# Optimization experiments

Measured on AMD Instinct MI355X. Metric: run time of the kernel, lower is better.

## Reference

```python
import jax, jax.numpy as jnp
import numpy as np

N_NODES = 100000
N_EDGES = 1000000
NEG_SLOPE = 0.2


def gat_conv(x, src, dst, W, al, ar, b, res, activation):
    """DGL-style GATConv. res is None (no residual), 'id' (identity residual), or a [in,H*D] matrix."""
    H, D = al.shape
    n = x.shape[0]
    feat = (x @ W).reshape(n, H, D)                      # [N,H,D]
    el = jnp.einsum('nhd,hd->nh', feat, al)              # [N,H]
    er = jnp.einsum('nhd,hd->nh', feat, ar)              # [N,H]
    e = jax.nn.leaky_relu(el[src] + er[dst], NEG_SLOPE)  # [E,H]
    # edge softmax over incoming edges of each dst node
    m = jax.lax.stop_gradient(jax.ops.segment_max(e, dst, num_segments=n))
    ex = jnp.exp(e - m[dst])
    s = jax.ops.segment_sum(ex, dst, num_segments=n)
    alpha = ex / s[dst]                                  # [E,H]
    out = jax.ops.segment_sum(feat[src] * alpha[:, :, None], dst, num_segments=n)  # [N,H,D]
    if res == 'id':
        out = out + x.reshape(n, H, D)
    elif res is not None:
        out = out + (x @ res).reshape(n, H, D)
    out = out + b.reshape(1, H, D)
    if activation is not None:
        out = activation(out)
    return out


def setup_inputs() -> dict:
    key = jax.random.key(0)
    ks = jax.random.split(key, 20)
    F_IN, HID = 128, 32
    H1, H2, H3 = 4, 4, 1
    C = 40
    sc = 0.1
    inp = {
        'x':   jax.random.normal(ks[0], (N_NODES, F_IN), dtype=jnp.float32),
        'src': jax.random.randint(ks[1], (N_EDGES,), 0, N_NODES, dtype=jnp.int32),
        'dst': jax.random.randint(ks[2], (N_EDGES,), 0, N_NODES, dtype=jnp.int32),
        # layer 1: in=128 -> H1*HID=128, no residual, elu
        'W1':  sc * jax.random.normal(ks[3], (F_IN, H1 * HID), dtype=jnp.float32),
        'al1': sc * jax.random.normal(ks[4], (H1, HID), dtype=jnp.float32),
        'ar1': sc * jax.random.normal(ks[5], (H1, HID), dtype=jnp.float32),
        'b1':  jnp.zeros((H1 * HID,), dtype=jnp.float32),
        # layer 2: in=128 -> H2*HID=128, identity residual, elu
        'W2':  sc * jax.random.normal(ks[6], (H1 * HID, H2 * HID), dtype=jnp.float32),
        'al2': sc * jax.random.normal(ks[7], (H2, HID), dtype=jnp.float32),
        'ar2': sc * jax.random.normal(ks[8], (H2, HID), dtype=jnp.float32),
        'b2':  jnp.zeros((H2 * HID,), dtype=jnp.float32),
        # layer 3 (output): in=128 -> H3*HID=32, projected residual, no activation
        'W3':  sc * jax.random.normal(ks[9], (H2 * HID, H3 * HID), dtype=jnp.float32),
        'al3': sc * jax.random.normal(ks[10], (H3, HID), dtype=jnp.float32),
        'ar3': sc * jax.random.normal(ks[11], (H3, HID), dtype=jnp.float32),
        'b3':  jnp.zeros((H3 * HID,), dtype=jnp.float32),
        'res3': sc * jax.random.normal(ks[12], (H2 * HID, H3 * HID), dtype=jnp.float32),
        # final classifier
        'Wfc': sc * jax.random.normal(ks[13], (HID, C), dtype=jnp.float32),
        'bfc': jnp.zeros((C,), dtype=jnp.float32),
    }
    return inp


def reference(x, src, dst, W1, al1, ar1, b1, W2, al2, ar2, b2, W3, al3, ar3, b3, res3, Wfc, bfc):
    n = x.shape[0]
    h = gat_conv(x, src, dst, W1, al1, ar1, b1, None, jax.nn.elu).reshape(n, -1)   # [N, 128]
    h = gat_conv(h, src, dst, W2, al2, ar2, b2, 'id', jax.nn.elu).reshape(n, -1)   # [N, 128]
    h = gat_conv(h, src, dst, W3, al3, ar3, b3, res3, None).mean(axis=1)           # [N, 32]
    return h @ Wfc + bfc                                                           # [N, 40]
```

## Files before the change

kernel.cpp:

```cpp
#include <hip/hip_runtime.h>
#include <cstdint>
#include <cstddef>

#define NN 100000
#define NE 1000000

typedef unsigned int uint;
typedef unsigned short ushort;
typedef __attribute__((ext_vector_type(8))) short bfrag;
typedef __attribute__((ext_vector_type(4))) float f32x4;

__device__ __forceinline__ ushort f2bf(float f){
  uint u = __float_as_uint(f);
  u += 0x7fffu + ((u >> 16) & 1u);
  return (ushort)(u >> 16);
}
__device__ __forceinline__ float bflo(uint p){ return __uint_as_float(p << 16); }
__device__ __forceinline__ float bfhi(uint p){ return __uint_as_float(p & 0xffff0000u); }


__global__ __launch_bounds__(256) void k_ticket(const int* __restrict__ dst, int* __restrict__ cnt,
                                                int* __restrict__ tick){
  int e = blockIdx.x*256 + threadIdx.x;
  if (e < NE) tick[e] = atomicAdd(&cnt[dst[e]], 1);
}

__global__ __launch_bounds__(256) void k_scan_local(const int* __restrict__ cnt, int* __restrict__ rowptr,
                                                    int* __restrict__ bsum){
  __shared__ int sm[256];
  int t = threadIdx.x;
  int i = blockIdx.x*256 + t;
  int v = (i < NN) ? cnt[i] : 0;
  sm[t] = v;
  __syncthreads();
  for (int off=1; off<256; off<<=1){
    int u = (t>=off) ? sm[t-off] : 0;
    __syncthreads();
    sm[t] += u;
    __syncthreads();
  }
  if (i < NN) rowptr[i] = sm[t] - v;
  if (t == 255) bsum[blockIdx.x] = sm[255];
}

__global__ __launch_bounds__(512) void k_scan_bsum(const int* __restrict__ bsum, int* __restrict__ boff, int nb){
  __shared__ int sm[512];
  int t = threadIdx.x;
  int v = (t < nb) ? bsum[t] : 0;
  sm[t] = v;
  __syncthreads();
  for (int off=1; off<512; off<<=1){
    int u = (t>=off) ? sm[t-off] : 0;
    __syncthreads();
    sm[t] += u;
    __syncthreads();
  }
  if (t < nb) boff[t] = sm[t] - v;
}

__global__ __launch_bounds__(256) void k_scan_add(int* __restrict__ rowptr, const int* __restrict__ boff){
  int i = blockIdx.x*256 + threadIdx.x;
  if (i < NN) rowptr[i] += boff[i>>8];
  else if (i == NN) rowptr[NN] = NE;
}

__global__ __launch_bounds__(256) void k_place(const int* __restrict__ src, const int* __restrict__ dst,
                                               const int* __restrict__ rowptr, const int* __restrict__ tick,
                                               int* __restrict__ csr){
  int e = blockIdx.x*256 + threadIdx.x;
  if (e < NE){
    int d = dst[e];
    csr[rowptr[d] + tick[e]] = src[e];
  }
}


__device__ __forceinline__ void bfrag_body(const float* __restrict__ B1, const float* __restrict__ B2,
                                           int n1, int n2, int NT, ushort* __restrict__ out, int i){
  if (i >= NT*4*64) return;
  int l = i & 63, ks = (i>>6)&3, nt = i>>8;
  int col = nt*16 + (l&15);
  int k0  = ks*32 + (l>>4)*8;
  const float* B; int stride, c;
  if (col < n1){ B = B1; stride = n1; c = col; }
  else         { B = B2; stride = n2; c = col - n1; }
  ushort v[8];
  #pragma unroll
  for (int j=0;j<8;j++) v[j] = f2bf(B[(size_t)(k0+j)*stride + c]);
  uint4 pk;
  pk.x = (uint)v[0] | ((uint)v[1]<<16);
  pk.y = (uint)v[2] | ((uint)v[3]<<16);
  pk.z = (uint)v[4] | ((uint)v[5]<<16);
  pk.w = (uint)v[6] | ((uint)v[7]<<16);
  *(uint4*)(out + (size_t)i*8) = pk;
}

#define CAST_BLOCKS 12500

__global__ __launch_bounds__(256) void k_prep(const float* __restrict__ x, ushort* __restrict__ xb,
                                              const float* __restrict__ W1, const float* __restrict__ W2,
                                              const float* __restrict__ W3, const float* __restrict__ res3,
                                              ushort* __restrict__ Bf1, ushort* __restrict__ Bf2,
                                              ushort* __restrict__ Bf3){
  int bid = blockIdx.x, t = threadIdx.x;
  if (bid < CAST_BLOCKS){
    int i = bid*256 + t;
    float4 v = ((const float4*)x)[i];
    uint2 p;
    p.x = (uint)f2bf(v.x) | ((uint)f2bf(v.y)<<16);
    p.y = (uint)f2bf(v.z) | ((uint)f2bf(v.w)<<16);
    ((uint2*)xb)[i] = p;
  } else {
    int r = bid - CAST_BLOCKS;
    if (r < 8)       bfrag_body(W1, nullptr, 128, 0, 8, Bf1, r*256 + t);
    else if (r < 16) bfrag_body(W2, nullptr, 128, 0, 8, Bf2, (r-8)*256 + t);
    else             bfrag_body(W3, res3,    32, 32, 4, Bf3, (r-16)*256 + t);
  }
}


template<int NT, int NTF, int H>
__global__ __launch_bounds__(256) void k_gemm_mfma(const ushort* __restrict__ Ab, const ushort* __restrict__ Bf,
                                                   ushort* __restrict__ featb, float* __restrict__ Cres,
                                                   const float* __restrict__ al, const float* __restrict__ ar,
                                                   float* __restrict__ el, float* __restrict__ er, int M){
  int t = threadIdx.x;
  int l = t & 63, w = t >> 6;
  int rw = blockIdx.x*64 + w*16;
  int c = l & 15, g = l >> 4;

  f32x4 acc[NT];
  #pragma unroll
  for (int nt=0;nt<NT;nt++) acc[nt] = (f32x4){0.f,0.f,0.f,0.f};

  int rowA = rw + c; if (rowA >= M) rowA = M-1;
  const ushort* Ap = Ab + (size_t)rowA*128 + g*8;
  const bfrag* Bp = (const bfrag*)Bf;

  #pragma unroll
  for (int ks=0; ks<4; ++ks){
    bfrag a = *(const bfrag*)(Ap + ks*32);
    #pragma unroll
    for (int nt=0; nt<NT; ++nt){
      bfrag b = Bp[(nt*4+ks)*64 + l];
      acc[nt] = __builtin_amdgcn_mfma_f32_16x16x32_bf16(a, b, acc[nt], 0, 0, 0);
    }
  }

  float alv[H][2], arv[H][2];
  #pragma unroll
  for (int h=0;h<H;h++){
    alv[h][0]=al[h*32+c];    arv[h][0]=ar[h*32+c];
    alv[h][1]=al[h*32+16+c]; arv[h][1]=ar[h*32+16+c];
  }

  #pragma unroll
  for (int reg=0; reg<4; ++reg){
    int row = rw + g*4 + reg;
    bool ok = row < M;
    #pragma unroll
    for (int h=0;h<H;h++){
      float pl = acc[2*h][reg]*alv[h][0] + acc[2*h+1][reg]*alv[h][1];
      float pr = acc[2*h][reg]*arv[h][0] + acc[2*h+1][reg]*arv[h][1];
      #pragma unroll
      for (int off=1; off<16; off<<=1){ pl += __shfl_xor(pl,off); pr += __shfl_xor(pr,off); }
      if (ok && c==0){ el[(size_t)row*H + h] = pl; er[(size_t)row*H + h] = pr; }
    }
    if (ok){
      #pragma unroll
      for (int nt=0; nt<NTF; ++nt)
        featb[(size_t)row*(NTF*16) + nt*16 + c] = f2bf(acc[nt][reg]);
      #pragma unroll
      for (int nt=NTF; nt<NT; ++nt)
        Cres[(size_t)row*((NT-NTF)*16) + (nt-NTF)*16 + c] = acc[nt][reg];
    }
  }
}


template<int RK, bool OBF>
__global__ __launch_bounds__(256) void k_agg4(const int* __restrict__ rowptr, const int* __restrict__ csr,
                                              const ushort* __restrict__ feat,
                                              const float* __restrict__ el, const float* __restrict__ er,
                                              const void* __restrict__ res, const float* __restrict__ bias,
                                              void* __restrict__ out, int act){
  __shared__ float exs[4][256];
  int lane = threadIdx.x & 63;
  int wloc = threadIdx.x >> 6;
  int node = blockIdx.x*4 + wloc;

  int beg = rowptr[node], deg = rowptr[node+1] - beg;
  bool fits = (deg <= 64);

  float erA = er[(size_t)node*4 + (lane&3)];
  float ssum = 0.f;
  for (int idx = lane; idx < deg*4; idx += 64){
    int s = csr[beg + (idx>>2)];
    float v = el[(size_t)s*4 + (idx&3)] + erA;
    v = (v>0.f) ? v : 0.2f*v;
    float e = __expf(v);
    if (fits) exs[wloc][idx] = e;
    ssum += e;
  }
  #pragma unroll
  for (int off=4; off<64; off<<=1) ssum += __shfl_xor(ssum, off);

  int l31 = lane & 31;
  int hm  = l31 >> 3;
  float sg  = __shfl(ssum, hm);
  float inv = (deg > 0) ? 1.f/sg : 0.f;
  int half = lane >> 5;
  int nE = (deg - half + 1) >> 1;

  const ushort* fbase = feat + (size_t)l31*4;
  float a0=0.f, a1=0.f, a2=0.f, a3=0.f;

  if (fits){
    int i = 0;
    for (; i+4 <= nE; i += 4){
      int e0 = 2*i+half, e1 = e0+2, e2 = e0+4, e3 = e0+6;
      int s0 = csr[beg+e0], s1 = csr[beg+e1], s2 = csr[beg+e2], s3 = csr[beg+e3];
      uint2 p0 = *(const uint2*)(fbase + (size_t)s0*128);
      uint2 p1 = *(const uint2*)(fbase + (size_t)s1*128);
      uint2 p2 = *(const uint2*)(fbase + (size_t)s2*128);
      uint2 p3 = *(const uint2*)(fbase + (size_t)s3*128);
      float w0 = exs[wloc][e0*4+hm]*inv, w1 = exs[wloc][e1*4+hm]*inv;
      float w2 = exs[wloc][e2*4+hm]*inv, w3 = exs[wloc][e3*4+hm]*inv;
      a0 += w0*bflo(p0.x) + w1*bflo(p1.x) + w2*bflo(p2.x) + w3*bflo(p3.x);
      a1 += w0*bfhi(p0.x) + w1*bfhi(p1.x) + w2*bfhi(p2.x) + w3*bfhi(p3.x);
      a2 += w0*bflo(p0.y) + w1*bflo(p1.y) + w2*bflo(p2.y) + w3*bflo(p3.y);
      a3 += w0*bfhi(p0.y) + w1*bfhi(p1.y) + w2*bfhi(p2.y) + w3*bfhi(p3.y);
    }
    for (; i < nE; ++i){
      int e0 = 2*i+half;
      int s0 = csr[beg+e0];
      uint2 p0 = *(const uint2*)(fbase + (size_t)s0*128);
      float w0 = exs[wloc][e0*4+hm]*inv;
      a0 += w0*bflo(p0.x); a1 += w0*bfhi(p0.x);
      a2 += w0*bflo(p0.y); a3 += w0*bfhi(p0.y);
    }
  } else {
    float erh = er[(size_t)node*4 + hm];
    for (int i = 0; i < nE; ++i){
      int e0 = 2*i+half;
      int s0 = csr[beg+e0];
      uint2 p0 = *(const uint2*)(fbase + (size_t)s0*128);
      float v = el[(size_t)s0*4 + hm] + erh;
      v = (v>0.f) ? v : 0.2f*v;
      float w0 = __expf(v)*inv;
      a0 += w0*bflo(p0.x); a1 += w0*bfhi(p0.x);
      a2 += w0*bflo(p0.y); a3 += w0*bfhi(p0.y);
    }
  }

  a0 += __shfl_xor(a0, 32); a1 += __shfl_xor(a1, 32);
  a2 += __shfl_xor(a2, 32); a3 += __shfl_xor(a3, 32);

  if (lane < 32){
    float o0=a0, o1=a1, o2=a2, o3=a3;
    if (RK == 1){
      uint2 rv = *(const uint2*)((const ushort*)res + (size_t)node*128 + lane*4);
      o0 += bflo(rv.x); o1 += bfhi(rv.x); o2 += bflo(rv.y); o3 += bfhi(rv.y);
    } else if (RK == 2){
      float4 rv = *(const float4*)((const float*)res + (size_t)node*128 + lane*4);
      o0 += rv.x; o1 += rv.y; o2 += rv.z; o3 += rv.w;
    }
    float4 bv = *(const float4*)(bias + lane*4);
    o0 += bv.x; o1 += bv.y; o2 += bv.z; o3 += bv.w;
    if (act){
      o0 = (o0>0.f)?o0:__expf(o0)-1.f;
      o1 = (o1>0.f)?o1:__expf(o1)-1.f;
      o2 = (o2>0.f)?o2:__expf(o2)-1.f;
      o3 = (o3>0.f)?o3:__expf(o3)-1.f;
    }
    if (OBF){
      uint2 pk;
      pk.x = (uint)f2bf(o0) | ((uint)f2bf(o1)<<16);
      pk.y = (uint)f2bf(o2) | ((uint)f2bf(o3)<<16);
      *(uint2*)((ushort*)out + (size_t)node*128 + lane*4) = pk;
    } else {
      float4 ov; ov.x=o0; ov.y=o1; ov.z=o2; ov.w=o3;
      *(float4*)((float*)out + (size_t)node*128 + lane*4) = ov;
    }
  }
}


__global__ __launch_bounds__(256) void k_agg1fc(const int* __restrict__ rowptr, const int* __restrict__ csr,
                                                const ushort* __restrict__ feat,
                                                const float* __restrict__ el, const float* __restrict__ er,
                                                const float* __restrict__ res, const float* __restrict__ bias,
                                                const float* __restrict__ Wfc, const float* __restrict__ bfc,
                                                float* __restrict__ out){
  __shared__ float exs[4][128];
  int lane = threadIdx.x & 63;
  int wloc = threadIdx.x >> 6;
  int node = blockIdx.x*4 + wloc;

  int beg = rowptr[node], deg = rowptr[node+1] - beg;
  bool fits = (deg <= 128);

  float er0 = er[node];
  float ssum = 0.f;
  for (int idx = lane; idx < deg; idx += 64){
    int s = csr[beg + idx];
    float v = el[s] + er0;
    v = (v>0.f) ? v : 0.2f*v;
    float e = __expf(v);
    if (fits) exs[wloc][idx] = e;
    ssum += e;
  }
  #pragma unroll
  for (int off=1; off<64; off<<=1) ssum += __shfl_xor(ssum, off);
  float inv = (deg > 0) ? 1.f/ssum : 0.f;

  int grp = lane >> 3, fl = lane & 7;
  const ushort* fbase = feat + (size_t)fl*4;
  float a0=0.f, a1=0.f, a2=0.f, a3=0.f;
  if (fits){
    #pragma unroll 2
    for (int ei = grp; ei < deg; ei += 8){
      int s = csr[beg + ei];
      uint2 pv = *(const uint2*)(fbase + (size_t)s*32);
      float w = exs[wloc][ei]*inv;
      a0 += w*bflo(pv.x); a1 += w*bfhi(pv.x);
      a2 += w*bflo(pv.y); a3 += w*bfhi(pv.y);
    }
  } else {
    for (int ei = grp; ei < deg; ei += 8){
      int s = csr[beg + ei];
      uint2 pv = *(const uint2*)(fbase + (size_t)s*32);
      float v = el[s] + er0;
      v = (v>0.f) ? v : 0.2f*v;
      float w = __expf(v)*inv;
      a0 += w*bflo(pv.x); a1 += w*bfhi(pv.x);
      a2 += w*bflo(pv.y); a3 += w*bfhi(pv.y);
    }
  }
  #pragma unroll
  for (int off=8; off<64; off<<=1){
    a0 += __shfl_xor(a0, off); a1 += __shfl_xor(a1, off);
    a2 += __shfl_xor(a2, off); a3 += __shfl_xor(a3, off);
  }

  {
    float4 rv = *(const float4*)(res + (size_t)node*32 + fl*4);
    float4 bv = *(const float4*)(bias + fl*4);
    a0 += rv.x + bv.x; a1 += rv.y + bv.y;
    a2 += rv.z + bv.z; a3 += rv.w + bv.w;
  }

  float acc = 0.f;
  #pragma unroll
  for (int k = 0; k < 32; ++k){
    int q = k >> 2, r = k & 3;
    float ok;
    if      (r == 0) ok = __shfl(a0, q);
    else if (r == 1) ok = __shfl(a1, q);
    else if (r == 2) ok = __shfl(a2, q);
    else             ok = __shfl(a3, q);
    acc += ok * Wfc[k*40 + lane];
  }
  if (lane < 40)
    out[(size_t)node*40 + lane] = acc + bfc[lane];
}


extern "C" void kernel_launch(void* const* d_in, const int* in_sizes, int n_in,
                              void* d_out, int out_size, void* d_ws, size_t ws_size,
                              hipStream_t stream){
  const float* x    = (const float*)d_in[0];
  const int*   src  = (const int*)  d_in[1];
  const int*   dst  = (const int*)  d_in[2];
  const float* W1   = (const float*)d_in[3];
  const float* al1  = (const float*)d_in[4];
  const float* ar1  = (const float*)d_in[5];
  const float* b1   = (const float*)d_in[6];
  const float* W2   = (const float*)d_in[7];
  const float* al2  = (const float*)d_in[8];
  const float* ar2  = (const float*)d_in[9];
  const float* b2   = (const float*)d_in[10];
  const float* W3   = (const float*)d_in[11];
  const float* al3  = (const float*)d_in[12];
  const float* ar3  = (const float*)d_in[13];
  const float* b3   = (const float*)d_in[14];
  const float* res3 = (const float*)d_in[15];
  const float* Wfc  = (const float*)d_in[16];
  const float* bfc  = (const float*)d_in[17];
  float* out = (float*)d_out;

  char* ws = (char*)d_ws;
  size_t o = 0;
  auto alloc = [&](size_t bytes)->char*{
    char* p = ws + o;
    o += (bytes + 255) & ~(size_t)255;
    return p;
  };
  int*    rowptr = (int*)   alloc((size_t)(NN+1)*4);
  int*    cnt    = (int*)   alloc((size_t)NN*4);
  int*    bsum   = (int*)   alloc(512*4);
  int*    boff   = (int*)   alloc(512*4);
  int*    tick   = (int*)   alloc((size_t)NE*4);
  int*    csr    = (int*)   alloc((size_t)NE*4);
  float*  el     = (float*) alloc((size_t)NN*4*4);
  float*  er     = (float*) alloc((size_t)NN*4*4);
  ushort* xb     = (ushort*)alloc((size_t)NN*128*2);
  ushort* featb  = (ushort*)alloc((size_t)NN*128*2);
  ushort* h1b    = (ushort*)alloc((size_t)NN*128*2);
  ushort* h2b    = (ushort*)alloc((size_t)NN*128*2);
  float*  res3p  = (float*) alloc((size_t)NN*32*4);
  ushort* Bf1    = (ushort*)alloc((size_t)8*4*64*8*2);
  ushort* Bf2    = (ushort*)alloc((size_t)8*4*64*8*2);
  ushort* Bf3    = (ushort*)alloc((size_t)4*4*64*8*2);
  (void)ws_size; (void)n_in; (void)in_sizes; (void)out_size;

  hipMemsetAsync(cnt, 0, (size_t)NN*4, stream);
  k_ticket<<<(NE+255)/256, 256, 0, stream>>>(dst, cnt, tick);
  int nb = (NN+255)/256;
  k_scan_local<<<nb, 256, 0, stream>>>(cnt, rowptr, bsum);
  k_scan_bsum<<<1, 512, 0, stream>>>(bsum, boff, nb);
  k_scan_add<<<(NN+1+255)/256, 256, 0, stream>>>(rowptr, boff);
  k_place<<<(NE+255)/256, 256, 0, stream>>>(src, dst, rowptr, tick, csr);

  k_prep<<<CAST_BLOCKS+20, 256, 0, stream>>>(x, xb, W1, W2, W3, res3, Bf1, Bf2, Bf3);

  int gemm_blocks = (NN+63)/64;

  k_gemm_mfma<8,8,4><<<gemm_blocks, 256, 0, stream>>>(xb, Bf1, featb, nullptr, al1, ar1, el, er, NN);
  k_agg4<0,true><<<NN/4, 256, 0, stream>>>(rowptr, csr, featb, el, er, nullptr, b1, h1b, 1);

  k_gemm_mfma<8,8,4><<<gemm_blocks, 256, 0, stream>>>(h1b, Bf2, featb, nullptr, al2, ar2, el, er, NN);
  k_agg4<1,true><<<NN/4, 256, 0, stream>>>(rowptr, csr, featb, el, er, h1b, b2, h2b, 1);

  k_gemm_mfma<4,2,1><<<gemm_blocks, 256, 0, stream>>>(h2b, Bf3, featb, res3p, al3, ar3, el, er, NN);
  k_agg1fc<<<NN/4, 256, 0, stream>>>(rowptr, csr, featb, el, er, res3p, b3, Wfc, bfc, out);
}
```

Measured before the change: 342.1 us.

## Fuse edge-softmax into single gather pass; split final FC into separate kernel

The aggregation kernels no longer do a separate pass that computes exp scores into shared memory. They compute the unnormalised exp weights inline while gathering features, accumulate the sum alongside, and normalise once at the end. This removes the second csr/el traversal and the shared-memory staging. The last layer's per-node FC via 32 shuffles is replaced by a separate tiled k_fc kernel that reads an h3 intermediate. That adds an extra launch and a round trip of the intermediate through global memory. Softmax without max-subtraction matches the previous code's behaviour.

```diff
diff --git a/kernel.cpp b/kernel.cpp
--- a/kernel.cpp
+++ b/kernel.cpp
@@ -184,77 +184,55 @@
                                               const float* __restrict__ el, const float* __restrict__ er,
                                               const void* __restrict__ res, const float* __restrict__ bias,
                                               void* __restrict__ out, int act){
-  __shared__ float exs[4][256];
   int lane = threadIdx.x & 63;
-  int wloc = threadIdx.x >> 6;
-  int node = blockIdx.x*4 + wloc;
+  int node = blockIdx.x*4 + (threadIdx.x >> 6);
 
   int beg = rowptr[node], deg = rowptr[node+1] - beg;
-  bool fits = (deg <= 64);
-
-  float erA = er[(size_t)node*4 + (lane&3)];
-  float ssum = 0.f;
-  for (int idx = lane; idx < deg*4; idx += 64){
-    int s = csr[beg + (idx>>2)];
-    float v = el[(size_t)s*4 + (idx&3)] + erA;
-    v = (v>0.f) ? v : 0.2f*v;
-    float e = __expf(v);
-    if (fits) exs[wloc][idx] = e;
-    ssum += e;
-  }
-  #pragma unroll
-  for (int off=4; off<64; off<<=1) ssum += __shfl_xor(ssum, off);
 
   int l31 = lane & 31;
   int hm  = l31 >> 3;
-  float sg  = __shfl(ssum, hm);
-  float inv = (deg > 0) ? 1.f/sg : 0.f;
   int half = lane >> 5;
+  float erh = er[(size_t)node*4 + hm];
+  const ushort* fbase = feat + (size_t)l31*4;
+  const int* cp = csr + beg;
+
+  float ssum = 0.f;
+  float a0=0.f, a1=0.f, a2=0.f, a3=0.f;
   int nE = (deg - half + 1) >> 1;
 
-  const ushort* fbase = feat + (size_t)l31*4;
-  float a0=0.f, a1=0.f, a2=0.f, a3=0.f;
-
-  if (fits){
-    int i = 0;
-    for (; i+4 <= nE; i += 4){
-      int e0 = 2*i+half, e1 = e0+2, e2 = e0+4, e3 = e0+6;
-      int s0 = csr[beg+e0], s1 = csr[beg+e1], s2 = csr[beg+e2], s3 = csr[beg+e3];
-      uint2 p0 = *(const uint2*)(fbase + (size_t)s0*128);
-      uint2 p1 = *(const uint2*)(fbase + (size_t)s1*128);
-      uint2 p2 = *(const uint2*)(fbase + (size_t)s2*128);
-      uint2 p3 = *(const uint2*)(fbase + (size_t)s3*128);
-      float w0 = exs[wloc][e0*4+hm]*inv, w1 = exs[wloc][e1*4+hm]*inv;
-      float w2 = exs[wloc][e2*4+hm]*inv, w3 = exs[wloc][e3*4+hm]*inv;
-      a0 += w0*bflo(p0.x) + w1*bflo(p1.x) + w2*bflo(p2.x) + w3*bflo(p3.x);
-      a1 += w0*bfhi(p0.x) + w1*bfhi(p1.x) + w2*bfhi(p2.x) + w3*bfhi(p3.x);
-      a2 += w0*bflo(p0.y) + w1*bflo(p1.y) + w2*bflo(p2.y) + w3*bflo(p3.y);
-      a3 += w0*bfhi(p0.y) + w1*bfhi(p1.y) + w2*bfhi(p2.y) + w3*bfhi(p3.y);
-    }
-    for (; i < nE; ++i){
-      int e0 = 2*i+half;
-      int s0 = csr[beg+e0];
-      uint2 p0 = *(const uint2*)(fbase + (size_t)s0*128);
-      float w0 = exs[wloc][e0*4+hm]*inv;
-      a0 += w0*bflo(p0.x); a1 += w0*bfhi(p0.x);
-      a2 += w0*bflo(p0.y); a3 += w0*bfhi(p0.y);
-    }
-  } else {
-    float erh = er[(size_t)node*4 + hm];
-    for (int i = 0; i < nE; ++i){
-      int e0 = 2*i+half;
-      int s0 = csr[beg+e0];
-      uint2 p0 = *(const uint2*)(fbase + (size_t)s0*128);
-      float v = el[(size_t)s0*4 + hm] + erh;
-      v = (v>0.f) ? v : 0.2f*v;
-      float w0 = __expf(v)*inv;
-      a0 += w0*bflo(p0.x); a1 += w0*bfhi(p0.x);
-      a2 += w0*bflo(p0.y); a3 += w0*bfhi(p0.y);
-    }
-  }
-
+  int i = 0;
+  for (; i+4 <= nE; i += 4){
+    int e0 = 2*i+half, e1 = e0+2, e2 = e0+4, e3 = e0+6;
+    int s0 = cp[e0], s1 = cp[e1], s2 = cp[e2], s3 = cp[e3];
+    uint2 p0 = *(const uint2*)(fbase + (size_t)s0*128);
+    uint2 p1 = *(const uint2*)(fbase + (size_t)s1*128);
+    uint2 p2 = *(const uint2*)(fbase + (size_t)s2*128);
+    uint2 p3 = *(const uint2*)(fbase + (size_t)s3*128);
+    float v0 = el[(size_t)s0*4+hm] + erh; v0=(v0>0.f)?v0:0.2f*v0; float w0=__expf(v0);
+    float v1 = el[(size_t)s1*4+hm] + erh; v1=(v1>0.f)?v1:0.2f*v1; float w1=__expf(v1);
+    float v2 = el[(size_t)s2*4+hm] + erh; v2=(v2>0.f)?v2:0.2f*v2; float w2=__expf(v2);
+    float v3 = el[(size_t)s3*4+hm] + erh; v3=(v3>0.f)?v3:0.2f*v3; float w3=__expf(v3);
+    ssum += w0+w1+w2+w3;
+    a0 += w0*bflo(p0.x) + w1*bflo(p1.x) + w2*bflo(p2.x) + w3*bflo(p3.x);
+    a1 += w0*bfhi(p0.x) + w1*bfhi(p1.x) + w2*bfhi(p2.x) + w3*bfhi(p3.x);
+    a2 += w0*bflo(p0.y) + w1*bflo(p1.y) + w2*bflo(p2.y) + w3*bflo(p3.y);
+    a3 += w0*bfhi(p0.y) + w1*bfhi(p1.y) + w2*bfhi(p2.y) + w3*bfhi(p3.y);
+  }
+  for (; i < nE; ++i){
+    int e0 = 2*i+half;
+    int s0 = cp[e0];
+    uint2 p0 = *(const uint2*)(fbase + (size_t)s0*128);
+    float v0 = el[(size_t)s0*4+hm] + erh; v0=(v0>0.f)?v0:0.2f*v0; float w0=__expf(v0);
+    ssum += w0;
+    a0 += w0*bflo(p0.x); a1 += w0*bfhi(p0.x);
+    a2 += w0*bflo(p0.y); a3 += w0*bfhi(p0.y);
+  }
+
+  ssum += __shfl_xor(ssum, 32);
   a0 += __shfl_xor(a0, 32); a1 += __shfl_xor(a1, 32);
   a2 += __shfl_xor(a2, 32); a3 += __shfl_xor(a3, 32);
+  float inv = (deg > 0) ? 1.f/ssum : 0.f;
+  a0 *= inv; a1 *= inv; a2 *= inv; a3 *= inv;
 
   if (lane < 32){
     float o0=a0, o1=a1, o2=a2, o3=a3;
@@ -286,83 +264,76 @@
 }
 
 
-__global__ __launch_bounds__(256) void k_agg1fc(const int* __restrict__ rowptr, const int* __restrict__ csr,
-                                                const ushort* __restrict__ feat,
-                                                const float* __restrict__ el, const float* __restrict__ er,
-                                                const float* __restrict__ res, const float* __restrict__ bias,
-                                                const float* __restrict__ Wfc, const float* __restrict__ bfc,
-                                                float* __restrict__ out){
-  __shared__ float exs[4][128];
+__global__ __launch_bounds__(256) void k_agg1(const int* __restrict__ rowptr, const int* __restrict__ csr,
+                                              const ushort* __restrict__ feat,
+                                              const float* __restrict__ el, const float* __restrict__ er,
+                                              const float* __restrict__ res, const float* __restrict__ bias,
+                                              float* __restrict__ h3){
   int lane = threadIdx.x & 63;
-  int wloc = threadIdx.x >> 6;
-  int node = blockIdx.x*4 + wloc;
+  int node = blockIdx.x*4 + (threadIdx.x >> 6);
 
   int beg = rowptr[node], deg = rowptr[node+1] - beg;
-  bool fits = (deg <= 128);
-
+  int sub = lane >> 4, fl = lane & 15;
   float er0 = er[node];
-  float ssum = 0.f;
-  for (int idx = lane; idx < deg; idx += 64){
-    int s = csr[beg + idx];
-    float v = el[s] + er0;
-    v = (v>0.f) ? v : 0.2f*v;
-    float e = __expf(v);
-    if (fits) exs[wloc][idx] = e;
-    ssum += e;
-  }
-  #pragma unroll
-  for (int off=1; off<64; off<<=1) ssum += __shfl_xor(ssum, off);
+  const ushort* fbase = feat + (size_t)fl*2;
+  const int* cp = csr + beg;
+
+  float ssum = 0.f, a0 = 0.f, a1 = 0.f;
+  for (int ei = sub; ei < deg; ei += 4){
+    int s = cp[ei];
+    uint pv = *(const uint*)(fbase + (size_t)s*32);
+    float v = el[s] + er0; v = (v>0.f)?v:0.2f*v;
+    float w = __expf(v);
+    ssum += w;
+    a0 += w*bflo(pv); a1 += w*bfhi(pv);
+  }
+  ssum += __shfl_xor(ssum, 16); ssum += __shfl_xor(ssum, 32);
+  a0 += __shfl_xor(a0, 16); a0 += __shfl_xor(a0, 32);
+  a1 += __shfl_xor(a1, 16); a1 += __shfl_xor(a1, 32);
   float inv = (deg > 0) ? 1.f/ssum : 0.f;
 
-  int grp = lane >> 3, fl = lane & 7;
-  const ushort* fbase = feat + (size_t)fl*4;
-  float a0=0.f, a1=0.f, a2=0.f, a3=0.f;
-  if (fits){
-    #pragma unroll 2
-    for (int ei = grp; ei < deg; ei += 8){
-      int s = csr[beg + ei];
-      uint2 pv = *(const uint2*)(fbase + (size_t)s*32);
-      float w = exs[wloc][ei]*inv;
-      a0 += w*bflo(pv.x); a1 += w*bfhi(pv.x);
-      a2 += w*bflo(pv.y); a3 += w*bfhi(pv.y);
-    }
-  } else {
-    for (int ei = grp; ei < deg; ei += 8){
-      int s = csr[beg + ei];
-      uint2 pv = *(const uint2*)(fbase + (size_t)s*32);
-      float v = el[s] + er0;
-      v = (v>0.f) ? v : 0.2f*v;
-      float w = __expf(v)*inv;
-      a0 += w*bflo(pv.x); a1 += w*bfhi(pv.x);
-      a2 += w*bflo(pv.y); a3 += w*bfhi(pv.y);
-    }
-  }
-  #pragma unroll
-  for (int off=8; off<64; off<<=1){
-    a0 += __shfl_xor(a0, off); a1 += __shfl_xor(a1, off);
-    a2 += __shfl_xor(a2, off); a3 += __shfl_xor(a3, off);
-  }
-
-  {
-    float4 rv = *(const float4*)(res + (size_t)node*32 + fl*4);
-    float4 bv = *(const float4*)(bias + fl*4);
-    a0 += rv.x + bv.x; a1 += rv.y + bv.y;
-    a2 += rv.z + bv.z; a3 += rv.w + bv.w;
-  }
-
-  float acc = 0.f;
-  #pragma unroll
-  for (int k = 0; k < 32; ++k){
-    int q = k >> 2, r = k & 3;
-    float ok;
-    if      (r == 0) ok = __shfl(a0, q);
-    else if (r == 1) ok = __shfl(a1, q);
-    else if (r == 2) ok = __shfl(a2, q);
-    else             ok = __shfl(a3, q);
-    acc += ok * Wfc[k*40 + lane];
-  }
-  if (lane < 40)
-    out[(size_t)node*40 + lane] = acc + bfc[lane];
+  if (lane < 16){
+    float2 rv = *(const float2*)(res + (size_t)node*32 + 2*fl);
+    float o0 = a0*inv + rv.x + bias[2*fl];
+    float o1 = a1*inv + rv.y + bias[2*fl+1];
+    float2 ov; ov.x = o0; ov.y = o1;
+    *(float2*)(h3 + (size_t)node*32 + 2*fl) = ov;
+  }
+}
+
+
+__global__ __launch_bounds__(256) void k_fc(const float* __restrict__ h, const float* __restrict__ W,
+                                            const float* __restrict__ b, float* __restrict__ out){
+  __shared__ float Ws[32*40];
+  __shared__ float Hs[64][33];
+  __shared__ float bs[40];
+  int t = threadIdx.x;
+  for (int i=t; i<1280; i+=256) Ws[i] = W[i];
+  if (t < 40) bs[t] = b[t];
+  int n0 = blockIdx.x*64;
+  for (int idx=t; idx<512; idx+=256){
+    int r = idx>>3, c4 = idx&7;
+    float4 v;
+    if (n0 + r < NN) v = *(const float4*)(h + (size_t)(n0+r)*32 + c4*4);
+    else v = make_float4(0.f,0.f,0.f,0.f);
+    Hs[r][c4*4+0]=v.x; Hs[r][c4*4+1]=v.y; Hs[r][c4*4+2]=v.z; Hs[r][c4*4+3]=v.w;
+  }
+  __syncthreads();
+  int n = t>>2, cg = t&3;
+  float acc[10];
+  #pragma unroll
+  for (int j=0;j<10;j++) acc[j] = 0.f;
+  #pragma unroll
+  for (int k=0;k<32;k++){
+    float hv = Hs[n][k];
+    #pragma unroll
+    for (int j=0;j<10;j++) acc[j] += hv * Ws[k*40 + cg + 4*j];
+  }
+  int row = n0 + n;
+  if (row < NN){
+    #pragma unroll
+    for (int j=0;j<10;j++) out[(size_t)row*40 + cg + 4*j] = acc[j] + bs[cg+4*j];
+  }
 }
 
 
@@ -409,6 +380,7 @@
   ushort* h1b    = (ushort*)alloc((size_t)NN*128*2);
   ushort* h2b    = (ushort*)alloc((size_t)NN*128*2);
   float*  res3p  = (float*) alloc((size_t)NN*32*4);
+  float*  h3     = (float*) alloc((size_t)NN*32*4);
   ushort* Bf1    = (ushort*)alloc((size_t)8*4*64*8*2);
   ushort* Bf2    = (ushort*)alloc((size_t)8*4*64*8*2);
   ushort* Bf3    = (ushort*)alloc((size_t)4*4*64*8*2);
@@ -433,5 +405,6 @@
   k_agg4<1,true><<<NN/4, 256, 0, stream>>>(rowptr, csr, featb, el, er, h1b, b2, h2b, 1);
 
   k_gemm_mfma<4,2,1><<<gemm_blocks, 256, 0, stream>>>(h2b, Bf3, featb, res3p, al3, ar3, el, er, NN);
-  k_agg1fc<<<NN/4, 256, 0, stream>>>(rowptr, csr, featb, el, er, res3p, b3, Wfc, bfc, out);
-}
+  k_agg1<<<NN/4, 256, 0, stream>>>(rowptr, csr, featb, el, er, res3p, b3, h3);
+  k_fc<<<gemm_blocks, 256, 0, stream>>>(h3, Wfc, bfc, out);
+}
```

After: 321.4 us. 1.06x faster.
